# Optimization experiments

Hardware: AMD Instinct MI355X
Metric: run time of the kernel (lower is better)

The kernel has to match this reference:

```python
import jax, jax.numpy as jnp
import numpy as np

EMB = 256   # EMB_SIZE hard-coded in source
H = 8       # num heads (all heads share the same Q/K/V, as in source)
DK = EMB // H  # 32
B, T = 16, 2048
LN_EPS = 1e-5


def _layernorm(a, g, b):
    m = jnp.mean(a, axis=-1, keepdims=True)
    v = jnp.mean(jnp.square(a - m), axis=-1, keepdims=True)
    return (a - m) * jax.lax.rsqrt(v + LN_EPS) * g + b


def setup_inputs() -> dict:
    key = jax.random.key(0)
    ks = jax.random.split(key, 8)
    sc = 0.02
    return {
        "x": jax.random.normal(ks[0], (B, T, EMB), jnp.float32),
        "Wq": jax.random.normal(ks[1], (EMB, DK), jnp.float32) * sc,
        "Wk": jax.random.normal(ks[2], (EMB, DK), jnp.float32) * sc,
        "Wv": jax.random.normal(ks[3], (EMB, DK), jnp.float32) * sc,
        "Wp": jax.random.normal(ks[4], (EMB, EMB), jnp.float32) * sc,
        "bp": jnp.zeros((EMB,), jnp.float32),
        "W1": jax.random.normal(ks[5], (EMB, 4 * EMB), jnp.float32) * sc,
        "b1": jnp.zeros((4 * EMB,), jnp.float32),
        "W2": jax.random.normal(ks[6], (4 * EMB, EMB), jnp.float32) * sc,
        "b2": jnp.zeros((EMB,), jnp.float32),
        "g1": jnp.ones((EMB,), jnp.float32),
        "be1": jnp.zeros((EMB,), jnp.float32),
        "g2": jnp.ones((EMB,), jnp.float32),
        "be2": jnp.zeros((EMB,), jnp.float32),
    }


def reference(x, Wq, Wk, Wv, Wp, bp, W1, b1, W2, b2, g1, be1, g2, be2):
    # Single shared-head QKV projections (bias-free), as in source
    q = x @ Wq  # [B,T,DK]
    k = x @ Wk
    v = x @ Wv
    # Causal self-attention with explicit score matrix [B,T,T]
    scores = jnp.einsum("btd,bsd->bts", q, k) / jnp.sqrt(jnp.float32(DK))
    causal = jnp.tril(jnp.ones((T, T), dtype=bool))
    scores = jnp.where(causal, scores, -jnp.inf)
    a = jax.nn.softmax(scores, axis=-1)
    attn = jnp.einsum("bts,bsd->btd", a, v)  # [B,T,DK]
    # Source concatenates h identical copies of the same attention output
    cat = jnp.tile(attn, (1, 1, H))  # [B,T,EMB]
    mh = cat @ Wp + bp
    y1 = _layernorm(x + mh, g1, be1)
    ff = jax.nn.gelu(y1 @ W1 + b1, approximate=False) @ W2 + b2
    return _layernorm(y1 + ff, g2, be2)
```

## Files before the change

kernel.cpp:

```cpp
#include <hip/hip_runtime.h>

#define BB 16
#define TT 2048
#define EE 256
#define DK 32
#define MM (BB*TT)
#define FF 1024

typedef __bf16 bf16_t;
typedef __bf16 bf16x8 __attribute__((ext_vector_type(8)));
typedef __bf16 bf16x4 __attribute__((ext_vector_type(4)));
typedef float  f32x4  __attribute__((ext_vector_type(4)));

__device__ __forceinline__ f32x4 mfma16(bf16x8 a, bf16x8 b, f32x4 c){
  return __builtin_amdgcn_mfma_f32_16x16x32_bf16(a, b, c, 0, 0, 0);
}
__device__ __forceinline__ void gload_lds16(const void* g, void* l){
  __builtin_amdgcn_global_load_lds((__attribute__((address_space(1))) void*)g,
                                   (__attribute__((address_space(3))) void*)l,
                                   16, 0, 0);
}

__launch_bounds__(256)
__global__ void prep_kernel(const float* __restrict__ Wq, const float* __restrict__ Wk,
                            const float* __restrict__ Wv, const float* __restrict__ Wp,
                            const float* __restrict__ W1, const float* __restrict__ W2,
                            bf16_t* __restrict__ wqkv, float* __restrict__ wpe,
                            bf16_t* __restrict__ w1t, bf16_t* __restrict__ w2t)
{
  const int i = blockIdx.x*256 + threadIdx.x;
  if (i < 96*256) {
    const int r = i >> 8, c = i & 255;
    float v;
    if (r < 32)      v = Wq[c*32 + r] * 0.17677669529663687f;
    else if (r < 64) v = Wk[c*32 + (r-32)];
    else             v = Wv[c*32 + (r-64)];
    wqkv[i] = (bf16_t)v;
  }
  if (i < 32*256) {
    const int d = i >> 8, n = i & 255;
    float s = 0.f;
    #pragma unroll
    for (int h = 0; h < 8; ++h) s += Wp[(h*32 + d)*256 + n];
    wpe[i] = s;
  }
  if (i < 1024*256) {
    const int n = i >> 8, k = i & 255;
    w1t[i] = (bf16_t)W1[(size_t)k*1024 + n];
  }
  if (i < 256*1024) {
    const int n = i >> 10, k = i & 1023;
    w2t[i] = (bf16_t)W2[(size_t)k*256 + n];
  }
}

__launch_bounds__(256)
__global__ void qkv_kernel(const float* __restrict__ x, const bf16_t* __restrict__ wqkv,
                           bf16_t* __restrict__ q, bf16_t* __restrict__ kd,
                           bf16_t* __restrict__ vT)
{
  __shared__ bf16_t Ws[96*256];
  const int tid = threadIdx.x;
  #pragma unroll
  for (int i = 0; i < 12; ++i) {
    const int v8  = tid + i*256;
    const int row = v8 >> 5;
    const int bir = (v8 & 31) * 16;
    *(bf16x8*)((char*)Ws + row*512 + (bir ^ ((row & 7) << 4))) =
        *(const bf16x8*)(wqkv + (size_t)v8*8);
  }
  __syncthreads();

  const int w = tid >> 6, l = tid & 63;
  const int lr = l & 15, lk4 = l >> 4, lkb = lk4*8;
  const int m0 = blockIdx.x * 64;
  const int arow = m0 + w*16 + lr;
  const float* xr = x + (size_t)arow * 256;

  f32x4 acc[6] = {};
  #pragma unroll
  for (int s = 0; s < 8; ++s) {
    const int kb = s*32 + lkb;
    const float4 v0 = *(const float4*)(xr + kb);
    const float4 v1 = *(const float4*)(xr + kb + 4);
    bf16x8 a;
    a[0]=(bf16_t)v0.x; a[1]=(bf16_t)v0.y; a[2]=(bf16_t)v0.z; a[3]=(bf16_t)v0.w;
    a[4]=(bf16_t)v1.x; a[5]=(bf16_t)v1.y; a[6]=(bf16_t)v1.z; a[7]=(bf16_t)v1.w;
    #pragma unroll
    for (int j = 0; j < 6; ++j) {
      const int nrow = j*16 + lr;
      const bf16x8 bf = *(const bf16x8*)((const char*)Ws + nrow*512 +
                                         ((kb*2) ^ ((nrow & 7) << 4)));
      acc[j] = mfma16(a, bf, acc[j]);
    }
  }
  #pragma unroll
  for (int j = 0; j < 6; ++j) {
    #pragma unroll
    for (int r = 0; r < 4; ++r) {
      const int orow = m0 + w*16 + lk4*4 + r;
      const int col  = j*16 + lr;
      const bf16_t v = (bf16_t)acc[j][r];
      if (col < 32)       q[(size_t)orow*32 + col] = v;
      else if (col < 64)  kd[(size_t)orow*32 + (col-32)] = v;
      else                vT[(((size_t)(orow >> 11))*32 + (col-64))*TT + (orow & 2047)] = v;
    }
  }
}

__launch_bounds__(256)
__global__ void attnp_kernel(const bf16_t* __restrict__ q, const bf16_t* __restrict__ kd,
                             const bf16_t* __restrict__ vT,
                             float* __restrict__ part_acc, float* __restrict__ part_ml)
{
  __shared__ bf16_t P[4][16*128];
  const int tid = threadIdx.x;
  const int w = tid >> 6, l = tid & 63;
  const int wv = blockIdx.x*4 + w;
  const int lr = l & 15, g4 = l >> 4;
  const float NEG_INF = -__builtin_inff();

  const int b = wv / 320;
  const int u = wv - b*320;
  int r, base;
  if      (u >= 192) { r = 3; base = 192; }
  else if (u >= 96)  { r = 2; base = 96;  }
  else if (u >= 32)  { r = 1; base = 32;  }
  else               { r = 0; base = 0;   }
  const int qq = u - base;
  const int g  = r*32 + qq / (r+1);
  const int c  = qq - (qq / (r+1))*(r+1);
  const int t_total = (g >> 3) + 1;
  const int t0 = c*4;
  const int t1 = min(t0 + 4, t_total);

  const bf16_t* qb = q  + (size_t)b*TT*32;
  const bf16_t* kb = kd + (size_t)b*TT*32;
  const bf16_t* vb = vT + (size_t)b*32*TT;
  const int q0 = g*16;
  const int qg = q0 + lr;

  const bf16x8 qa = *(const bf16x8*)(qb + (size_t)(q0 + lr)*32 + g4*8);
  const bf16_t* v0r = vb + (size_t)lr*TT;
  const bf16_t* v1r = vb + (size_t)(16 + lr)*TT;

  f32x4 acc0 = {0.f,0.f,0.f,0.f}, acc1 = {0.f,0.f,0.f,0.f};
  float mrun = NEG_INF, lsum = 0.f;
  char* pb = (char*)&P[w][0];
  const int swz = (lr & 7) << 4;
  const f32x4 zf = {0.f,0.f,0.f,0.f};

  for (int t = t0; t < t1; ++t) {
    const int k0 = t * 128;
    f32x4 s[8];
    #pragma unroll
    for (int cc = 0; cc < 8; ++cc) {
      const bf16x8 kf = *(const bf16x8*)(kb + (size_t)(k0 + cc*16 + lr)*32 + g4*8);
      s[cc] = mfma16(kf, qa, zf);
    }
    if (t == t_total - 1) {
      #pragma unroll
      for (int cc = 0; cc < 8; ++cc)
        #pragma unroll
        for (int rr = 0; rr < 4; ++rr)
          if (k0 + cc*16 + g4*4 + rr > qg) s[cc][rr] = NEG_INF;
    }
    float mt = NEG_INF;
    #pragma unroll
    for (int cc = 0; cc < 8; ++cc) {
      float a01 = fmaxf(s[cc][0], s[cc][1]), a23 = fmaxf(s[cc][2], s[cc][3]);
      mt = fmaxf(mt, fmaxf(a01, a23));
    }
    mt = fmaxf(mt, __shfl_xor(mt, 16));
    mt = fmaxf(mt, __shfl_xor(mt, 32));
    const float mn = fmaxf(mrun, mt);
    const float sc = __expf(mrun - mn);
    float ps = 0.f;
    #pragma unroll
    for (int cc = 0; cc < 8; ++cc) {
      float p0 = __expf(s[cc][0]-mn), p1 = __expf(s[cc][1]-mn);
      float p2 = __expf(s[cc][2]-mn), p3 = __expf(s[cc][3]-mn);
      s[cc][0]=p0; s[cc][1]=p1; s[cc][2]=p2; s[cc][3]=p3;
      ps += (p0+p1) + (p2+p3);
    }
    ps += __shfl_xor(ps, 16);
    ps += __shfl_xor(ps, 32);
    lsum = lsum*sc + ps;
    mrun = mn;
    acc0 *= sc; acc1 *= sc;
    #pragma unroll
    for (int cc = 0; cc < 8; ++cc) {
      bf16x4 pk;
      pk[0]=(bf16_t)s[cc][0]; pk[1]=(bf16_t)s[cc][1];
      pk[2]=(bf16_t)s[cc][2]; pk[3]=(bf16_t)s[cc][3];
      *(bf16x4*)(pb + lr*256 + ((cc*32 + g4*8) ^ swz)) = pk;
    }
    #pragma unroll
    for (int h = 0; h < 4; ++h) {
      const bf16x8 pbf = *(const bf16x8*)(pb + lr*256 + ((h*64 + g4*16) ^ swz));
      acc0 = mfma16(*(const bf16x8*)(v0r + k0 + h*32 + g4*8), pbf, acc0);
      acc1 = mfma16(*(const bf16x8*)(v1r + k0 + h*32 + g4*8), pbf, acc1);
    }
  }
  float* pa = part_acc + (size_t)wv*512;
  *(f32x4*)(pa + l*8)     = acc0;
  *(f32x4*)(pa + l*8 + 4) = acc1;
  if (l < 16) {
    part_ml[wv*32 + l]      = mrun;
    part_ml[wv*32 + 16 + l] = lsum;
  }
}

__launch_bounds__(256)
__global__ void attnc_kernel(const float* __restrict__ part_acc,
                             const float* __restrict__ part_ml,
                             bf16_t* __restrict__ attn)
{
  const int tid = threadIdx.x;
  const int id = blockIdx.x*4 + (tid >> 6);
  const int l = tid & 63, lr = l & 15, g4 = l >> 4;
  const int b = id >> 7, g = id & 127;
  const int r = g >> 5;
  const int base = (r == 0) ? 0 : (r == 1) ? 32 : (r == 2) ? 96 : 192;
  const int p0 = b*320 + base + (g - (r << 5))*(r + 1);
  const int nc = r + 1;
  const float NEG_INF = -__builtin_inff();

  float m0v=NEG_INF,m1v=NEG_INF,m2v=NEG_INF,m3v=NEG_INF;
  float l0v=0,l1v=0,l2v=0,l3v=0;
  f32x4 a00={0,0,0,0},a01={0,0,0,0},a10={0,0,0,0},a11={0,0,0,0};
  f32x4 a20={0,0,0,0},a21={0,0,0,0},a30={0,0,0,0},a31={0,0,0,0};
  {
    const float* pa = part_acc + (size_t)p0*512;
    a00 = *(const f32x4*)(pa + l*8); a01 = *(const f32x4*)(pa + l*8 + 4);
    m0v = part_ml[p0*32 + lr]; l0v = part_ml[p0*32 + 16 + lr];
  }
  if (nc > 1) {
    const float* pa = part_acc + (size_t)(p0+1)*512;
    a10 = *(const f32x4*)(pa + l*8); a11 = *(const f32x4*)(pa + l*8 + 4);
    m1v = part_ml[(p0+1)*32 + lr]; l1v = part_ml[(p0+1)*32 + 16 + lr];
  }
  if (nc > 2) {
    const float* pa = part_acc + (size_t)(p0+2)*512;
    a20 = *(const f32x4*)(pa + l*8); a21 = *(const f32x4*)(pa + l*8 + 4);
    m2v = part_ml[(p0+2)*32 + lr]; l2v = part_ml[(p0+2)*32 + 16 + lr];
  }
  if (nc > 3) {
    const float* pa = part_acc + (size_t)(p0+3)*512;
    a30 = *(const f32x4*)(pa + l*8); a31 = *(const f32x4*)(pa + l*8 + 4);
    m3v = part_ml[(p0+3)*32 + lr]; l3v = part_ml[(p0+3)*32 + 16 + lr];
  }
  const float M = fmaxf(fmaxf(m0v, m1v), fmaxf(m2v, m3v));
  const float w0 = __expf(m0v - M), w1 = __expf(m1v - M);
  const float w2 = __expf(m2v - M), w3 = __expf(m3v - M);
  const float L = l0v*w0 + l1v*w1 + l2v*w2 + l3v*w3;
  const float inv = 1.0f / L;
  f32x4 o0 = (a00*w0 + a10*w1 + a20*w2 + a30*w3) * inv;
  f32x4 o1 = (a01*w0 + a11*w1 + a21*w2 + a31*w3) * inv;

  bf16_t* ao = attn + ((size_t)b*TT + g*16 + lr)*32;
  bf16x4 ob0, ob1;
  ob0[0]=(bf16_t)o0[0]; ob0[1]=(bf16_t)o0[1]; ob0[2]=(bf16_t)o0[2]; ob0[3]=(bf16_t)o0[3];
  ob1[0]=(bf16_t)o1[0]; ob1[1]=(bf16_t)o1[1]; ob1[2]=(bf16_t)o1[2]; ob1[3]=(bf16_t)o1[3];
  *(bf16x4*)(ao + g4*4)      = ob0;
  *(bf16x4*)(ao + 16 + g4*4) = ob1;
}

__launch_bounds__(256)
__global__ void ln1_kernel(const float* __restrict__ x, const bf16_t* __restrict__ attn,
                           const float* __restrict__ wpe, const float* __restrict__ bp,
                           const float* __restrict__ g1, const float* __restrict__ be1,
                           bf16_t* __restrict__ y1b)
{
  __shared__ float Wp_s[32*256];
  const int tid = threadIdx.x;
  for (int i = tid; i < 32*64; i += 256)
    ((float4*)Wp_s)[i] = ((const float4*)wpe)[i];
  __syncthreads();

  const int w = tid >> 6, l = tid & 63;
  const int n = l * 4;
  const float4 gv  = *(const float4*)(g1  + n);
  const float4 bev = *(const float4*)(be1 + n);
  const float4 bpv = *(const float4*)(bp  + n);

  #pragma unroll 1
  for (int it = 0; it < 8; ++it) {
    const int row = blockIdx.x*32 + it*4 + w;
    const bf16_t* ar = attn + (size_t)row*32;
    float a[32];
    #pragma unroll
    for (int i = 0; i < 4; ++i) {
      const bf16x8 t = *(const bf16x8*)(ar + i*8);
      #pragma unroll
      for (int j = 0; j < 8; ++j) a[i*8 + j] = (float)t[j];
    }
    float mh[4] = {bpv.x, bpv.y, bpv.z, bpv.w};
    #pragma unroll
    for (int d = 0; d < 32; ++d) {
      const float4 wv = *(const float4*)(Wp_s + d*256 + n);
      const float ad = a[d];
      mh[0] = fmaf(ad, wv.x, mh[0]); mh[1] = fmaf(ad, wv.y, mh[1]);
      mh[2] = fmaf(ad, wv.z, mh[2]); mh[3] = fmaf(ad, wv.w, mh[3]);
    }
    const float4 xv = *(const float4*)(x + (size_t)row*256 + n);
    const float t0 = xv.x + mh[0], t1 = xv.y + mh[1];
    const float t2 = xv.z + mh[2], t3 = xv.w + mh[3];
    float s1 = (t0+t1) + (t2+t3);
    float s2 = (t0*t0 + t1*t1) + (t2*t2 + t3*t3);
    #pragma unroll
    for (int m = 1; m < 64; m <<= 1) { s1 += __shfl_xor(s1, m); s2 += __shfl_xor(s2, m); }
    const float mean = s1 * (1.0f/256.0f);
    const float var  = s2 * (1.0f/256.0f) - mean*mean;
    const float rs   = rsqrtf(var + 1e-5f);
    float4 yv;
    yv.x = (t0-mean)*rs*gv.x + bev.x; yv.y = (t1-mean)*rs*gv.y + bev.y;
    yv.z = (t2-mean)*rs*gv.z + bev.z; yv.w = (t3-mean)*rs*gv.w + bev.w;
    bf16x4 yb; yb[0]=(bf16_t)yv.x; yb[1]=(bf16_t)yv.y; yb[2]=(bf16_t)yv.z; yb[3]=(bf16_t)yv.w;
    *(bf16x4*)(y1b + (size_t)row*256 + n) = yb;
  }
}

__launch_bounds__(256)
__global__ void ff1_kernel(const bf16_t* __restrict__ A, const bf16_t* __restrict__ Bt,
                           const float* __restrict__ b1, bf16_t* __restrict__ H)
{
  __shared__ bf16_t As[2][128*64];
  __shared__ bf16_t Bs[2][128*64];
  const int tid = threadIdx.x;
  const int w = tid >> 6, l = tid & 63;
  const int m0 = blockIdx.x * 128, n0 = blockIdx.y * 128;
  const int wm = (w >> 1) * 64, wn = (w & 1) * 64;
  const int lr = l & 15, lk4 = l >> 4;
  const int srow = l >> 3;
  const int scol = ((l & 7) ^ srow) * 8;
  const bf16_t* Ab = A  + (size_t)m0*256 + scol;
  const bf16_t* Bb = Bt + (size_t)n0*256 + scol;

  f32x4 acc[4][4] = {};

  #define FF1_STAGE(t, d)                                                     \
    { const int k0_ = (t)*64;                                                 \
      _Pragma("unroll")                                                       \
      for (int i_ = 0; i_ < 4; ++i_) {                                        \
        const int r0_ = w*32 + i_*8;                                          \
        gload_lds16(Ab + (size_t)(r0_ + srow)*256 + k0_, (char*)As[d] + r0_*128); \
        gload_lds16(Bb + (size_t)(r0_ + srow)*256 + k0_, (char*)Bs[d] + r0_*128); \
      } }

  FF1_STAGE(0, 0);
  __syncthreads();
  for (int t = 0; t < 4; ++t) {
    if (t < 3) FF1_STAGE(t+1, (t+1)&1);
    const char* as = (const char*)As[t&1];
    const char* bs = (const char*)Bs[t&1];
    #pragma unroll
    for (int kk = 0; kk < 2; ++kk) {
      bf16x8 af[4], bf[4];
      #pragma unroll
      for (int i = 0; i < 4; ++i) {
        const int row = wm + i*16 + lr;
        af[i] = *(const bf16x8*)(as + row*128 + ((kk*64 + lk4*16) ^ ((row & 7) << 4)));
      }
      #pragma unroll
      for (int j = 0; j < 4; ++j) {
        const int row = wn + j*16 + lr;
        bf[j] = *(const bf16x8*)(bs + row*128 + ((kk*64 + lk4*16) ^ ((row & 7) << 4)));
      }
      #pragma unroll
      for (int i = 0; i < 4; ++i)
        #pragma unroll
        for (int j = 0; j < 4; ++j)
          acc[i][j] = mfma16(af[i], bf[j], acc[i][j]);
    }
    __syncthreads();
  }
  #undef FF1_STAGE

  #pragma unroll
  for (int i = 0; i < 4; ++i)
    #pragma unroll
    for (int r = 0; r < 4; ++r) {
      const int row = m0 + wm + i*16 + lk4*4 + r;
      #pragma unroll
      for (int j = 0; j < 4; ++j) {
        const int col = n0 + wn + j*16 + lr;
        const float v = acc[i][j][r] + b1[col];
        const float z = 1.5957691216057308f * v * fmaf(0.044715f, v*v, 1.0f);
        const float gg = v * __builtin_amdgcn_rcpf(1.0f + __expf(-z));
        H[(size_t)row*FF + col] = (bf16_t)gg;
      }
    }
}

__launch_bounds__(512)
__global__ void ff2_kernel(const bf16_t* __restrict__ A, const bf16_t* __restrict__ Bt,
                           const float* __restrict__ b2, const bf16_t* __restrict__ y1b,
                           const float* __restrict__ g2, const float* __restrict__ be2,
                           float* __restrict__ out)
{
  __shared__ bf16_t As[2][128*64];
  __shared__ bf16_t Bs[2][256*64];
  __shared__ float red[128*8];
  const int tid = threadIdx.x;
  const int w = tid >> 6, l = tid & 63;
  const int m0 = blockIdx.x * 128;
  const int wm = (w >> 2) * 64, wn = (w & 3) * 64;
  const int lr = l & 15, lk4 = l >> 4;
  const int srow = l >> 3;
  const int scol = ((l & 7) ^ srow) * 8;
  const bf16_t* Ab = A + (size_t)m0*FF + scol;
  const bf16_t* Bb = Bt + scol;

  f32x4 acc[4][4] = {};

  #define FF2_STAGE(t, d)                                                     \
    { const int k0_ = (t)*64;                                                 \
      _Pragma("unroll")                                                       \
      for (int i_ = 0; i_ < 2; ++i_) {                                        \
        const int r0_ = w*16 + i_*8;                                          \
        gload_lds16(Ab + (size_t)(r0_ + srow)*FF + k0_, (char*)As[d] + r0_*128); \
      }                                                                       \
      _Pragma("unroll")                                                       \
      for (int i_ = 0; i_ < 4; ++i_) {                                        \
        const int r0_ = w*32 + i_*8;                                          \
        gload_lds16(Bb + (size_t)(r0_ + srow)*FF + k0_, (char*)Bs[d] + r0_*128); \
      } }

  FF2_STAGE(0, 0);
  __syncthreads();
  for (int t = 0; t < 16; ++t) {
    if (t < 15) FF2_STAGE(t+1, (t+1)&1);
    const char* as = (const char*)As[t&1];
    const char* bs = (const char*)Bs[t&1];
    #pragma unroll
    for (int kk = 0; kk < 2; ++kk) {
      bf16x8 af[4], bf[4];
      #pragma unroll
      for (int i = 0; i < 4; ++i) {
        const int row = wm + i*16 + lr;
        af[i] = *(const bf16x8*)(as + row*128 + ((kk*64 + lk4*16) ^ ((row & 7) << 4)));
      }
      #pragma unroll
      for (int j = 0; j < 4; ++j) {
        const int row = wn + j*16 + lr;
        bf[j] = *(const bf16x8*)(bs + row*128 + ((kk*64 + lk4*16) ^ ((row & 7) << 4)));
      }
      #pragma unroll
      for (int i = 0; i < 4; ++i)
        #pragma unroll
        for (int j = 0; j < 4; ++j)
          acc[i][j] = mfma16(af[i], bf[j], acc[i][j]);
    }
    __syncthreads();
  }
  #undef FF2_STAGE

  #pragma unroll
  for (int i = 0; i < 4; ++i)
    #pragma unroll
    for (int j = 0; j < 4; ++j) {
      const int col = wn + j*16 + lr;
      #pragma unroll
      for (int r = 0; r < 4; ++r) {
        const int row = m0 + wm + i*16 + lk4*4 + r;
        acc[i][j][r] += b2[col] + (float)y1b[(size_t)row*256 + col];
      }
    }
  #pragma unroll
  for (int i = 0; i < 4; ++i)
    #pragma unroll
    for (int r = 0; r < 4; ++r) {
      float s1 = (acc[i][0][r] + acc[i][1][r]) + (acc[i][2][r] + acc[i][3][r]);
      float s2 = (acc[i][0][r]*acc[i][0][r] + acc[i][1][r]*acc[i][1][r]) +
                 (acc[i][2][r]*acc[i][2][r] + acc[i][3][r]*acc[i][3][r]);
      #pragma unroll
      for (int m = 1; m < 16; m <<= 1) { s1 += __shfl_xor(s1, m); s2 += __shfl_xor(s2, m); }
      if (lr == 0) {
        const int rl = wm + i*16 + lk4*4 + r;
        red[rl*8 + (w & 3)*2]     = s1;
        red[rl*8 + (w & 3)*2 + 1] = s2;
      }
    }
  __syncthreads();
  #pragma unroll
  for (int i = 0; i < 4; ++i)
    #pragma unroll
    for (int r = 0; r < 4; ++r) {
      const int rl = wm + i*16 + lk4*4 + r;
      const float S1 = (red[rl*8+0] + red[rl*8+2]) + (red[rl*8+4] + red[rl*8+6]);
      const float S2 = (red[rl*8+1] + red[rl*8+3]) + (red[rl*8+5] + red[rl*8+7]);
      const float mean = S1 * (1.0f/256.0f);
      const float var  = S2 * (1.0f/256.0f) - mean*mean;
      const float rs   = rsqrtf(var + 1e-5f);
      #pragma unroll
      for (int j = 0; j < 4; ++j) {
        const int col = wn + j*16 + lr;
        out[(size_t)(m0 + rl)*256 + col] = (acc[i][j][r] - mean)*rs*g2[col] + be2[col];
      }
    }
}

extern "C" void kernel_launch(void* const* d_in, const int* in_sizes, int n_in,
                              void* d_out, int out_size, void* d_ws, size_t ws_size,
                              hipStream_t stream)
{
  const float* x   = (const float*)d_in[0];
  const float* Wq  = (const float*)d_in[1];
  const float* Wk  = (const float*)d_in[2];
  const float* Wv  = (const float*)d_in[3];
  const float* Wp  = (const float*)d_in[4];
  const float* bp  = (const float*)d_in[5];
  const float* W1  = (const float*)d_in[6];
  const float* b1  = (const float*)d_in[7];
  const float* W2  = (const float*)d_in[8];
  const float* b2  = (const float*)d_in[9];
  const float* g1  = (const float*)d_in[10];
  const float* be1 = (const float*)d_in[11];
  const float* g2  = (const float*)d_in[12];
  const float* be2 = (const float*)d_in[13];

  char* ws = (char*)d_ws;
  bf16_t* qd   = (bf16_t*)(ws + ((size_t)0  << 20));
  bf16_t* kd   = (bf16_t*)(ws + ((size_t)2  << 20));
  bf16_t* vTd  = (bf16_t*)(ws + ((size_t)4  << 20));
  bf16_t* attn = (bf16_t*)(ws + ((size_t)6  << 20));
  bf16_t* y1b  = (bf16_t*)(ws + ((size_t)8  << 20));
  bf16_t* h1   = (bf16_t*)(ws + ((size_t)24 << 20));
  bf16_t* wqkv = (bf16_t*)(ws + ((size_t)88 << 20));
  float*  wpe  = (float*) (ws + ((size_t)89 << 20));
  bf16_t* w1t  = (bf16_t*)(ws + ((size_t)90 << 20));
  bf16_t* w2t  = (bf16_t*)(ws + ((size_t)91 << 20));
  float*  pml  = (float*) (ws + ((size_t)92 << 20));
  float*  pacc = (float*) (ws + ((size_t)93 << 20));
  float* out = (float*)d_out;

  prep_kernel<<<1024, 256, 0, stream>>>(Wq, Wk, Wv, Wp, W1, W2, wqkv, wpe, w1t, w2t);
  qkv_kernel<<<512, 256, 0, stream>>>(x, wqkv, qd, kd, vTd);
  attnp_kernel<<<1280, 256, 0, stream>>>(qd, kd, vTd, pacc, pml);
  attnc_kernel<<<512, 256, 0, stream>>>(pacc, pml, attn);
  ln1_kernel<<<1024, 256, 0, stream>>>(x, attn, wpe, bp, g1, be1, y1b);
  ff1_kernel<<<dim3(256, 8), 256, 0, stream>>>(y1b, w1t, b1, h1);
  ff2_kernel<<<256, 512, 0, stream>>>(h1, w2t, b2, y1b, g2, be2, out);
}
```

Before: 149.2 us.

## Drop LDS double buffering in FF GEMMs and halve FF2 row tile

```diff
diff --git a/kernel.cpp b/kernel.cpp
--- a/kernel.cpp
+++ b/kernel.cpp
@@ -325,8 +325,8 @@
 __global__ void ff1_kernel(const bf16_t* __restrict__ A, const bf16_t* __restrict__ Bt,
                            const float* __restrict__ b1, bf16_t* __restrict__ H)
 {
-  __shared__ bf16_t As[2][128*64];
-  __shared__ bf16_t Bs[2][128*64];
+  __shared__ bf16_t As[128*64];
+  __shared__ bf16_t Bs[128*64];
   const int tid = threadIdx.x;
   const int w = tid >> 6, l = tid & 63;
   const int m0 = blockIdx.x * 128, n0 = blockIdx.y * 128;
@@ -339,33 +339,29 @@
 
   f32x4 acc[4][4] = {};
 
-  #define FF1_STAGE(t, d)                                                     \
-    { const int k0_ = (t)*64;                                                 \
-      _Pragma("unroll")                                                       \
-      for (int i_ = 0; i_ < 4; ++i_) {                                        \
-        const int r0_ = w*32 + i_*8;                                          \
-        gload_lds16(Ab + (size_t)(r0_ + srow)*256 + k0_, (char*)As[d] + r0_*128); \
-        gload_lds16(Bb + (size_t)(r0_ + srow)*256 + k0_, (char*)Bs[d] + r0_*128); \
-      } }
-
-  FF1_STAGE(0, 0);
-  __syncthreads();
   for (int t = 0; t < 4; ++t) {
-    if (t < 3) FF1_STAGE(t+1, (t+1)&1);
-    const char* as = (const char*)As[t&1];
-    const char* bs = (const char*)Bs[t&1];
+    const int k0 = t*64;
+    #pragma unroll
+    for (int i_ = 0; i_ < 4; ++i_) {
+      const int r0_ = w*32 + i_*8;
+      gload_lds16(Ab + (size_t)(r0_ + srow)*256 + k0, (char*)As + r0_*128);
+      gload_lds16(Bb + (size_t)(r0_ + srow)*256 + k0, (char*)Bs + r0_*128);
+    }
+    __syncthreads();
     #pragma unroll
     for (int kk = 0; kk < 2; ++kk) {
       bf16x8 af[4], bf[4];
       #pragma unroll
       for (int i = 0; i < 4; ++i) {
         const int row = wm + i*16 + lr;
-        af[i] = *(const bf16x8*)(as + row*128 + ((kk*64 + lk4*16) ^ ((row & 7) << 4)));
+        af[i] = *(const bf16x8*)((const char*)As + row*128 +
+                                 ((kk*64 + lk4*16) ^ ((row & 7) << 4)));
       }
       #pragma unroll
       for (int j = 0; j < 4; ++j) {
         const int row = wn + j*16 + lr;
-        bf[j] = *(const bf16x8*)(bs + row*128 + ((kk*64 + lk4*16) ^ ((row & 7) << 4)));
+        bf[j] = *(const bf16x8*)((const char*)Bs + row*128 +
+                                 ((kk*64 + lk4*16) ^ ((row & 7) << 4)));
       }
       #pragma unroll
       for (int i = 0; i < 4; ++i)
@@ -375,7 +371,6 @@
     }
     __syncthreads();
   }
-  #undef FF1_STAGE
 
   #pragma unroll
   for (int i = 0; i < 4; ++i)
@@ -399,65 +394,59 @@
                            const float* __restrict__ g2, const float* __restrict__ be2,
                            float* __restrict__ out)
 {
-  __shared__ bf16_t As[2][128*64];
-  __shared__ bf16_t Bs[2][256*64];
-  __shared__ float red[128*8];
+  __shared__ bf16_t As[64*64];
+  __shared__ bf16_t Bs[256*64];
+  __shared__ float red[64*8];
   const int tid = threadIdx.x;
   const int w = tid >> 6, l = tid & 63;
-  const int m0 = blockIdx.x * 128;
-  const int wm = (w >> 2) * 64, wn = (w & 3) * 64;
+  const int m0 = blockIdx.x * 64;
+  const int wm = (w >> 2) * 32, wn = (w & 3) * 64;
   const int lr = l & 15, lk4 = l >> 4;
   const int srow = l >> 3;
   const int scol = ((l & 7) ^ srow) * 8;
   const bf16_t* Ab = A + (size_t)m0*FF + scol;
   const bf16_t* Bb = Bt + scol;
 
-  f32x4 acc[4][4] = {};
-
-  #define FF2_STAGE(t, d)                                                     \
-    { const int k0_ = (t)*64;                                                 \
-      _Pragma("unroll")                                                       \
-      for (int i_ = 0; i_ < 2; ++i_) {                                        \
-        const int r0_ = w*16 + i_*8;                                          \
-        gload_lds16(Ab + (size_t)(r0_ + srow)*FF + k0_, (char*)As[d] + r0_*128); \
-      }                                                                       \
-      _Pragma("unroll")                                                       \
-      for (int i_ = 0; i_ < 4; ++i_) {                                        \
-        const int r0_ = w*32 + i_*8;                                          \
-        gload_lds16(Bb + (size_t)(r0_ + srow)*FF + k0_, (char*)Bs[d] + r0_*128); \
-      } }
-
-  FF2_STAGE(0, 0);
-  __syncthreads();
+  f32x4 acc[2][4] = {};
+
   for (int t = 0; t < 16; ++t) {
-    if (t < 15) FF2_STAGE(t+1, (t+1)&1);
-    const char* as = (const char*)As[t&1];
-    const char* bs = (const char*)Bs[t&1];
+    const int k0 = t*64;
+    {
+      const int r0_ = w*8;
+      gload_lds16(Ab + (size_t)(r0_ + srow)*FF + k0, (char*)As + r0_*128);
+    }
+    #pragma unroll
+    for (int i_ = 0; i_ < 4; ++i_) {
+      const int r0_ = w*32 + i_*8;
+      gload_lds16(Bb + (size_t)(r0_ + srow)*FF + k0, (char*)Bs + r0_*128);
+    }
+    __syncthreads();
     #pragma unroll
     for (int kk = 0; kk < 2; ++kk) {
-      bf16x8 af[4], bf[4];
-      #pragma unroll
-      for (int i = 0; i < 4; ++i) {
+      bf16x8 af[2], bf[4];
+      #pragma unroll
+      for (int i = 0; i < 2; ++i) {
         const int row = wm + i*16 + lr;
-        af[i] = *(const bf16x8*)(as + row*128 + ((kk*64 + lk4*16) ^ ((row & 7) << 4)));
+        af[i] = *(const bf16x8*)((const char*)As + row*128 +
+                                 ((kk*64 + lk4*16) ^ ((row & 7) << 4)));
       }
       #pragma unroll
       for (int j = 0; j < 4; ++j) {
         const int row = wn + j*16 + lr;
-        bf[j] = *(const bf16x8*)(bs + row*128 + ((kk*64 + lk4*16) ^ ((row & 7) << 4)));
-      }
-      #pragma unroll
-      for (int i = 0; i < 4; ++i)
+        bf[j] = *(const bf16x8*)((const char*)Bs + row*128 +
+                                 ((kk*64 + lk4*16) ^ ((row & 7) << 4)));
+      }
+      #pragma unroll
+      for (int i = 0; i < 2; ++i)
         #pragma unroll
         for (int j = 0; j < 4; ++j)
           acc[i][j] = mfma16(af[i], bf[j], acc[i][j]);
     }
     __syncthreads();
   }
-  #undef FF2_STAGE
-
-  #pragma unroll
-  for (int i = 0; i < 4; ++i)
+
+  #pragma unroll
+  for (int i = 0; i < 2; ++i)
     #pragma unroll
     for (int j = 0; j < 4; ++j) {
       const int col = wn + j*16 + lr;
@@ -468,7 +457,7 @@
       }
     }
   #pragma unroll
-  for (int i = 0; i < 4; ++i)
+  for (int i = 0; i < 2; ++i)
     #pragma unroll
     for (int r = 0; r < 4; ++r) {
       float s1 = (acc[i][0][r] + acc[i][1][r]) + (acc[i][2][r] + acc[i][3][r]);
@@ -484,7 +473,7 @@
     }
   __syncthreads();
   #pragma unroll
-  for (int i = 0; i < 4; ++i)
+  for (int i = 0; i < 2; ++i)
     #pragma unroll
     for (int r = 0; r < 4; ++r) {
       const int rl = wm + i*16 + lk4*4 + r;
@@ -541,5 +530,5 @@
   attnc_kernel<<<512, 256, 0, stream>>>(pacc, pml, attn);
   ln1_kernel<<<1024, 256, 0, stream>>>(x, attn, wpe, bp, g1, be1, y1b);
   ff1_kernel<<<dim3(256, 8), 256, 0, stream>>>(y1b, w1t, b1, h1);
-  ff2_kernel<<<256, 512, 0, stream>>>(h1, w2t, b2, y1b, g2, be2, out);
-}
+  ff2_kernel<<<512, 512, 0, stream>>>(h1, w2t, b2, y1b, g2, be2, out);
+}
```

After: 147.7 us. Within noise of the previous version (-1.1%).
